# Performance work log

Measured on AMD Instinct MI355X. Metric: run time of the kernel, lower is better.

## Reference

```python
import jax, jax.numpy as jnp
import numpy as np

B = 4_194_304  # batch rows


def _linear_params(key, fan_in, fan_out):
    # torch nn.Linear init: U(-1/sqrt(fan_in), 1/sqrt(fan_in)) for both W and b
    kw, kb = jax.random.split(key)
    bound = 1.0 / np.sqrt(fan_in)
    W = jax.random.uniform(kw, (fan_out, fan_in), jnp.float32, -bound, bound)
    b = jax.random.uniform(kb, (fan_out,), jnp.float32, -bound, bound)
    return W, b


def setup_inputs() -> dict:
    key = jax.random.key(0)
    keys = jax.random.split(key, 12)
    x = jax.random.normal(keys[0], (B, 8), jnp.float32)
    dims = [(8, 6), (6, 6), (6, 6), (6, 6), (6, 6), (6, 6), (6, 4), (4, 4), (4, 4), (4, 4), (4, 1)]
    inp = {"x": x}
    for i, (fi, fo) in enumerate(dims):
        W, b = _linear_params(keys[i + 1], fi, fo)
        inp[f"W{i+1}"] = W
        inp[f"b{i+1}"] = b
    return inp


def reference(x, W1, b1, W2, b2, W3, b3, W4, b4, W5, b5, W6, b6,
              W7, b7, W8, b8, W9, b9, W10, b10, W11, b11):
    h = x
    for W, b in ((W1, b1), (W2, b2), (W3, b3), (W4, b4), (W5, b5), (W6, b6),
                 (W7, b7), (W8, b8), (W9, b9), (W10, b10), (W11, b11)):
        h = jax.nn.sigmoid(h @ W.T + b)
    return h  # [B, 1]
```

## Files before the change

### kernel.cpp

```cpp
#include <hip/hip_runtime.h>


__device__ __forceinline__ float sigp(float z) {
    float u = z * z;
    float p = fmaf(u, -5.19503e-5f, 1.44971e-3f);
    p = fmaf(u, p, -0.0198386f);
    p = fmaf(u, p, 0.2497094f);
    return fmaf(z, p, 0.5f);
}

template <int FI, int FO, bool CLAMP>
__device__ __forceinline__ void layer(const float* __restrict__ h, float* __restrict__ o,
                                      const float* __restrict__ W,
                                      const float* __restrict__ b) {
#pragma unroll
    for (int j = 0; j < FO; ++j) {
        float acc = b[j];
#pragma unroll
        for (int i = 0; i < FI; ++i) acc = fmaf(h[i], W[j * FI + i], acc);
        if (CLAMP) acc = __builtin_amdgcn_fmed3f(acc, -3.0f, 3.0f);
        o[j] = sigp(acc);
    }
}

__global__ __launch_bounds__(256) void mlp11_f32(
    const float* __restrict__ x,
    const float* __restrict__ W1,  const float* __restrict__ b1,
    const float* __restrict__ W2,  const float* __restrict__ b2,
    const float* __restrict__ W3,  const float* __restrict__ b3,
    const float* __restrict__ W4,  const float* __restrict__ b4,
    const float* __restrict__ W5,  const float* __restrict__ b5,
    const float* __restrict__ W6,  const float* __restrict__ b6,
    const float* __restrict__ W7,  const float* __restrict__ b7,
    const float* __restrict__ W8,  const float* __restrict__ b8,
    const float* __restrict__ W9,  const float* __restrict__ b9,
    const float* __restrict__ W10, const float* __restrict__ b10,
    const float* __restrict__ W11, const float* __restrict__ b11,
    float* __restrict__ out, int nrows) {
    int row = blockIdx.x * 256 + (int)threadIdx.x;
    if (row >= nrows) return;

    const float4* xv = reinterpret_cast<const float4*>(x) + (size_t)row * 2;
    float4 a = xv[0];
    float4 c = xv[1];

    float h0[8] = {a.x, a.y, a.z, a.w, c.x, c.y, c.z, c.w};
    float h1[8];

    layer<8, 6, true >(h0, h1, W1, b1);
    layer<6, 6, false>(h1, h0, W2, b2);
    layer<6, 6, false>(h0, h1, W3, b3);
    layer<6, 6, false>(h1, h0, W4, b4);
    layer<6, 6, false>(h0, h1, W5, b5);
    layer<6, 6, false>(h1, h0, W6, b6);
    layer<6, 4, false>(h0, h1, W7, b7);
    layer<4, 4, false>(h1, h0, W8, b8);
    layer<4, 4, false>(h0, h1, W9, b9);
    layer<4, 4, false>(h1, h0, W10, b10);

    float acc = b11[0];
#pragma unroll
    for (int i = 0; i < 4; ++i) acc = fmaf(h0[i], W11[i], acc);
    out[row] = sigp(acc);
}

extern "C" void kernel_launch(void* const* d_in, const int* in_sizes, int n_in,
                              void* d_out, int out_size, void* d_ws, size_t ws_size,
                              hipStream_t stream) {
    const float* x = (const float*)d_in[0];
    const float* W[11];
    const float* b[11];
    for (int i = 0; i < 11; ++i) {
        W[i] = (const float*)d_in[1 + 2 * i];
        b[i] = (const float*)d_in[2 + 2 * i];
    }
    float* out = (float*)d_out;
    int nrows = in_sizes[0] / 8;

    int blocks = (nrows + 255) / 256;
    mlp11_f32<<<blocks, 256, 0, stream>>>(
        x,
        W[0], b[0], W[1], b[1], W[2], b[2], W[3], b[3], W[4], b[4],
        W[5], b[5], W[6], b[6], W[7], b[7], W[8], b[8], W[9], b[9],
        W[10], b[10],
        out, nrows);
}
```

Before: 56.28 us.

## Use grid-stride persistent loop with software prefetch of next row

```diff
diff --git a/kernel.cpp b/kernel.cpp
--- a/kernel.cpp
+++ b/kernel.cpp
@@ -23,8 +23,8 @@
     }
 }
 
-__global__ __launch_bounds__(256) void mlp11_f32(
-    const float* __restrict__ x,
+__device__ __forceinline__ float mlp_row(
+    const float4& a, const float4& c,
     const float* __restrict__ W1,  const float* __restrict__ b1,
     const float* __restrict__ W2,  const float* __restrict__ b2,
     const float* __restrict__ W3,  const float* __restrict__ b3,
@@ -35,15 +35,7 @@
     const float* __restrict__ W8,  const float* __restrict__ b8,
     const float* __restrict__ W9,  const float* __restrict__ b9,
     const float* __restrict__ W10, const float* __restrict__ b10,
-    const float* __restrict__ W11, const float* __restrict__ b11,
-    float* __restrict__ out, int nrows) {
-    int row = blockIdx.x * 256 + (int)threadIdx.x;
-    if (row >= nrows) return;
-
-    const float4* xv = reinterpret_cast<const float4*>(x) + (size_t)row * 2;
-    float4 a = xv[0];
-    float4 c = xv[1];
-
+    const float* __restrict__ W11, const float* __restrict__ b11) {
     float h0[8] = {a.x, a.y, a.z, a.w, c.x, c.y, c.z, c.w};
     float h1[8];
 
@@ -61,7 +53,50 @@
     float acc = b11[0];
 #pragma unroll
     for (int i = 0; i < 4; ++i) acc = fmaf(h0[i], W11[i], acc);
-    out[row] = sigp(acc);
+    return sigp(acc);
+}
+
+__global__ __launch_bounds__(256) void mlp11_f32(
+    const float* __restrict__ x,
+    const float* __restrict__ W1,  const float* __restrict__ b1,
+    const float* __restrict__ W2,  const float* __restrict__ b2,
+    const float* __restrict__ W3,  const float* __restrict__ b3,
+    const float* __restrict__ W4,  const float* __restrict__ b4,
+    const float* __restrict__ W5,  const float* __restrict__ b5,
+    const float* __restrict__ W6,  const float* __restrict__ b6,
+    const float* __restrict__ W7,  const float* __restrict__ b7,
+    const float* __restrict__ W8,  const float* __restrict__ b8,
+    const float* __restrict__ W9,  const float* __restrict__ b9,
+    const float* __restrict__ W10, const float* __restrict__ b10,
+    const float* __restrict__ W11, const float* __restrict__ b11,
+    float* __restrict__ out, int nrows) {
+    const int stride = (int)gridDim.x * 256;
+    int row = (int)blockIdx.x * 256 + (int)threadIdx.x;
+    if (row >= nrows) return;
+
+    const float4* __restrict__ xv = reinterpret_cast<const float4*>(x);
+
+    float4 a = xv[(size_t)row * 2];
+    float4 c = xv[(size_t)row * 2 + 1];
+
+    for (;;) {
+        int next = row + stride;
+        bool has_next = next < nrows;
+
+        float4 an, cn;
+        if (has_next) {
+            an = xv[(size_t)next * 2];
+            cn = xv[(size_t)next * 2 + 1];
+        }
+
+        out[row] = mlp_row(a, c, W1, b1, W2, b2, W3, b3, W4, b4, W5, b5,
+                           W6, b6, W7, b7, W8, b8, W9, b9, W10, b10, W11, b11);
+
+        if (!has_next) break;
+        row = next;
+        a = an;
+        c = cn;
+    }
 }
 
 extern "C" void kernel_launch(void* const* d_in, const int* in_sizes, int n_in,
@@ -78,6 +113,7 @@
     int nrows = in_sizes[0] / 8;
 
     int blocks = (nrows + 255) / 256;
+    if (blocks > 2048) blocks = 2048;
     mlp11_f32<<<blocks, 256, 0, stream>>>(
         x,
         W[0], b[0], W[1], b[1], W[2], b[2], W[3], b[3], W[4], b[4],
```

Result: slower. 113.3 us (+101.4%).
